# Performance work log

Hardware: AMD Instinct MI355X
Metric: run time of the kernel (lower is better)

## Reference

```python
import jax, jax.numpy as jnp
import numpy as np

HIDDEN = 1024
HEADS = 16
HEAD_DIM = HIDDEN // HEADS
FF = 4 * HIDDEN
B, S = 2, 2048


def _linear_params(key, out_dim, in_dim):
    kw, kb = jax.random.split(key)
    bound = 1.0 / np.sqrt(in_dim)
    W = jax.random.uniform(kw, (out_dim, in_dim), jnp.float32, -bound, bound)
    b = jax.random.uniform(kb, (out_dim,), jnp.float32, -bound, bound)
    return W, b


def setup_inputs() -> dict:
    key = jax.random.key(0)
    ks = jax.random.split(key, 8)
    x = jax.random.normal(ks[0], (B, S, HIDDEN), jnp.float32)
    attention_mask = jnp.ones((B, S), jnp.float32)
    Wq, bq = _linear_params(ks[1], HIDDEN, HIDDEN)
    Wk, bk = _linear_params(ks[2], HIDDEN, HIDDEN)
    Wv, bv = _linear_params(ks[3], HIDDEN, HIDDEN)
    Wo, bo = _linear_params(ks[4], HIDDEN, HIDDEN)
    W1, b1 = _linear_params(ks[5], FF, HIDDEN)
    W2, b2 = _linear_params(ks[6], HIDDEN, FF)
    g1 = jnp.ones((HIDDEN,), jnp.float32); be1 = jnp.zeros((HIDDEN,), jnp.float32)
    g2 = jnp.ones((HIDDEN,), jnp.float32); be2 = jnp.zeros((HIDDEN,), jnp.float32)
    return dict(x=x, attention_mask=attention_mask,
                Wq=Wq, bq=bq, Wk=Wk, bk=bk, Wv=Wv, bv=bv, Wo=Wo, bo=bo,
                W1=W1, b1=b1, W2=W2, b2=b2,
                g1=g1, be1=be1, g2=g2, be2=be2)


def _layer_norm(x, g, b, eps=1e-5):
    mu = jnp.mean(x, axis=-1, keepdims=True)
    var = jnp.mean(jnp.square(x - mu), axis=-1, keepdims=True)
    return (x - mu) * jax.lax.rsqrt(var + eps) * g + b


def reference(x, attention_mask, Wq, bq, Wk, bk, Wv, bv, Wo, bo,
              W1, b1, W2, b2, g1, be1, g2, be2):
    # Dropout is identity (eval mode / deterministic reference).
    residual = x
    h = _layer_norm(x, g1, be1)
    # [B,S,H] -> [B,nH,S,dh]
    def heads(t):
        return t.reshape(B, S, HEADS, HEAD_DIM).transpose(0, 2, 1, 3)
    q = heads(h @ Wq.T + bq)
    k = heads(h @ Wk.T + bk)
    v = heads(h @ Wv.T + bv)
    scores = jnp.einsum('bhqd,bhkd->bhqk', q, k) / np.sqrt(HEAD_DIM).astype(np.float32)
    scores = scores + (attention_mask[:, None, None, :] - 1.0) * 10000.0
    attn = jax.nn.softmax(scores, axis=-1)
    ctx = jnp.einsum('bhqk,bhkd->bhqd', attn, v)
    ctx = ctx.transpose(0, 2, 1, 3).reshape(B, S, HIDDEN)
    attn_out = ctx @ Wo.T + bo
    x = residual + attn_out
    residual = x
    h = _layer_norm(x, g2, be2)
    h = jax.nn.gelu(h @ W1.T + b1, approximate=False)
    h = h @ W2.T + b2
    return residual + h
```

## Files before the change

kernel.cpp:

```cpp
#include <hip/hip_runtime.h>
#include <hip/hip_bf16.h>
#include <math.h>

typedef __bf16 bf16;
typedef __bf16 bf16x4v __attribute__((ext_vector_type(4)));
typedef __bf16 bf16x8 __attribute__((ext_vector_type(8)));
typedef float  f32x4  __attribute__((ext_vector_type(4)));

#define HIDDEN 1024
#define TOKENS 4096
#define FFDIM  4096
#define SEQ    2048
#define NHEAD  16

#define LOG2E 1.44269504088896340736f

__device__ __forceinline__ void async_copy16(bf16* lds, const bf16* g)
{
    __builtin_amdgcn_global_load_lds(
        (__attribute__((address_space(1))) void*)g,
        (__attribute__((address_space(3))) void*)lds,
        16, 0, 0);
}

__global__ __launch_bounds__(256) void cvt_all_kernel(const float* __restrict__ wq,
    const float* __restrict__ wk, const float* __restrict__ wv, const float* __restrict__ wo,
    const float* __restrict__ w1, const float* __restrict__ w2, bf16* __restrict__ out)
{
    size_t i = ((size_t)blockIdx.x * 256 + threadIdx.x) * 4;
    int sel = (int)(i >> 20);
    const float* src;
    size_t off;
    if (sel < 4) { src = (sel == 0) ? wq : (sel == 1) ? wk : (sel == 2) ? wv : wo; off = i & ((1u << 20) - 1); }
    else if (sel < 8) { src = w1; off = i - ((size_t)4 << 20); }
    else              { src = w2; off = i - ((size_t)8 << 20); }
    float4 v = *(const float4*)&src[off];
    bf16x4v o = { (bf16)v.x, (bf16)v.y, (bf16)v.z, (bf16)v.w };
    *(bf16x4v*)&out[i] = o;
}

__global__ __launch_bounds__(256) void concat_bias_kernel(const float* __restrict__ bq,
    const float* __restrict__ bk, const float* __restrict__ bv, float* __restrict__ o)
{
    int i = blockIdx.x * 256 + threadIdx.x;
    float v = (i < 1024) ? bq[i] : (i < 2048 ? bk[i - 1024] : bv[i - 2048]);
    o[i] = v;
}

__global__ __launch_bounds__(256) void ln_kernel(const float* __restrict__ in,
    const float* __restrict__ g, const float* __restrict__ be, bf16* __restrict__ out)
{
    int row = blockIdx.x;
    int tid = threadIdx.x;
    const float* x = in + (size_t)row * HIDDEN;
    int i0 = tid * 4;
    float4 v = *(const float4*)&x[i0];
    float s  = v.x + v.y + v.z + v.w;
    float s2 = v.x*v.x + v.y*v.y + v.z*v.z + v.w*v.w;
    #pragma unroll
    for (int off = 32; off > 0; off >>= 1) { s += __shfl_xor(s, off); s2 += __shfl_xor(s2, off); }
    __shared__ float red[2][4];
    int wave = tid >> 6;
    if ((tid & 63) == 0) { red[0][wave] = s; red[1][wave] = s2; }
    __syncthreads();
    float ts  = red[0][0] + red[0][1] + red[0][2] + red[0][3];
    float ts2 = red[1][0] + red[1][1] + red[1][2] + red[1][3];
    float mu   = ts  * (1.0f / HIDDEN);
    float var  = ts2 * (1.0f / HIDDEN) - mu * mu;
    float rstd = rsqrtf(var + 1e-5f);
    float4 gg = *(const float4*)&g[i0];
    float4 bb = *(const float4*)&be[i0];
    bf16x4v o;
    o[0] = (bf16)((v.x - mu) * rstd * gg.x + bb.x);
    o[1] = (bf16)((v.y - mu) * rstd * gg.y + bb.y);
    o[2] = (bf16)((v.z - mu) * rstd * gg.z + bb.z);
    o[3] = (bf16)((v.w - mu) * rstd * gg.w + bb.w);
    *(bf16x4v*)&out[(size_t)row * HIDDEN + i0] = o;
}

template<int BM, int EPI, typename OT>
__global__ __launch_bounds__(256) void gemm_bt(const bf16* __restrict__ A, const bf16* __restrict__ Bt,
    const float* __restrict__ bias, const float* __restrict__ res, OT* __restrict__ C,
    int M, int N, int K)
{
    constexpr int MT = BM / 32;
    __shared__ bf16 As[BM * 64];
    __shared__ bf16 Bs[128 * 64];
    int tid  = threadIdx.x;
    int wave = tid >> 6, lane = tid & 63;
    int lm = lane & 15, quad = lane >> 4;
    int m0 = blockIdx.x * BM, n0 = blockIdx.y * 128;
    int wm = (wave >> 1) * (MT * 16), wn = (wave & 1) * 64;
    int r8 = lane >> 3, c8 = lane & 7;
    int gsw = (c8 ^ (r8 & 7)) * 8;
    f32x4 acc[MT][4] = {};
    for (int k0 = 0; k0 < K; k0 += 64) {
        #pragma unroll
        for (int ch = wave; ch < BM / 8; ch += 4)
            async_copy16(As + ch * 512, &A[(size_t)(m0 + ch * 8 + r8) * K + k0 + gsw]);
        #pragma unroll
        for (int ch = wave; ch < 16; ch += 4)
            async_copy16(Bs + ch * 512, &Bt[(size_t)(n0 + ch * 8 + r8) * K + k0 + gsw]);
        __syncthreads();
        bf16x8 af[MT][2], bfr[4][2];
        #pragma unroll
        for (int ks = 0; ks < 2; ks++) {
            int co = ((ks * 4 + quad) ^ (lm & 7)) * 8;
            #pragma unroll
            for (int t = 0; t < MT; t++) af[t][ks]  = *(const bf16x8*)&As[(wm + t * 16 + lm) * 64 + co];
            #pragma unroll
            for (int t = 0; t < 4; t++)  bfr[t][ks] = *(const bf16x8*)&Bs[(wn + t * 16 + lm) * 64 + co];
        }
        #pragma unroll
        for (int mt = 0; mt < MT; mt++)
            #pragma unroll
            for (int nt = 0; nt < 4; nt++)
                #pragma unroll
                for (int ks = 0; ks < 2; ks++)
                    acc[mt][nt] = __builtin_amdgcn_mfma_f32_16x16x32_bf16(af[mt][ks], bfr[nt][ks], acc[mt][nt], 0, 0, 0);
        __syncthreads();
    }
    #pragma unroll
    for (int mt = 0; mt < MT; mt++) {
        #pragma unroll
        for (int nt = 0; nt < 4; nt++) {
            int col = n0 + wn + nt * 16 + lm;
            float bv = bias[col];
            #pragma unroll
            for (int r = 0; r < 4; r++) {
                int row = m0 + wm + mt * 16 + quad * 4 + r;
                float vv = acc[mt][nt][r] + bv;
                if (EPI == 1) vv = 0.5f * vv * (1.0f + erff(vv * 0.70710678118654752f));
                if (EPI == 2) vv += res[(size_t)row * N + col];
                C[(size_t)row * N + col] = (OT)vv;
            }
        }
    }
}

__global__ __launch_bounds__(256) void gemm_qkv(const bf16* __restrict__ A, const bf16* __restrict__ W,
    const float* __restrict__ bias, bf16* __restrict__ qb, bf16* __restrict__ kb, bf16* __restrict__ vt)
{
    constexpr int K = HIDDEN;
    __shared__ bf16 As[128 * 64];
    __shared__ bf16 Bs[128 * 64];
    int tid  = threadIdx.x;
    int wave = tid >> 6, lane = tid & 63;
    int lm = lane & 15, quad = lane >> 4;
    int m0 = blockIdx.x * 128, n0 = blockIdx.y * 128;
    int wm = (wave >> 1) * 64, wn = (wave & 1) * 64;
    int r8 = lane >> 3, c8 = lane & 7;
    int gsw = (c8 ^ (r8 & 7)) * 8;
    f32x4 acc[4][4] = {};
    for (int k0 = 0; k0 < K; k0 += 64) {
        #pragma unroll
        for (int ch = wave; ch < 16; ch += 4) {
            async_copy16(As + ch * 512, &A[(size_t)(m0 + ch * 8 + r8) * K + k0 + gsw]);
            async_copy16(Bs + ch * 512, &W[(size_t)(n0 + ch * 8 + r8) * K + k0 + gsw]);
        }
        __syncthreads();
        bf16x8 af[4][2], bfr[4][2];
        #pragma unroll
        for (int ks = 0; ks < 2; ks++) {
            int co = ((ks * 4 + quad) ^ (lm & 7)) * 8;
            #pragma unroll
            for (int t = 0; t < 4; t++) {
                af[t][ks]  = *(const bf16x8*)&As[(wm + t * 16 + lm) * 64 + co];
                bfr[t][ks] = *(const bf16x8*)&Bs[(wn + t * 16 + lm) * 64 + co];
            }
        }
        #pragma unroll
        for (int mt = 0; mt < 4; mt++)
            #pragma unroll
            for (int nt = 0; nt < 4; nt++)
                #pragma unroll
                for (int ks = 0; ks < 2; ks++)
                    acc[mt][nt] = __builtin_amdgcn_mfma_f32_16x16x32_bf16(af[mt][ks], bfr[nt][ks], acc[mt][nt], 0, 0, 0);
        __syncthreads();
    }
    int region = n0 >> 10;
    #pragma unroll
    for (int mt = 0; mt < 4; mt++) {
        #pragma unroll
        for (int nt = 0; nt < 4; nt++) {
            int col = n0 + wn + nt * 16 + lm;
            float bv = bias[col];
            int cl = col & 1023;
            #pragma unroll
            for (int r = 0; r < 4; r++) {
                int row = m0 + wm + mt * 16 + quad * 4 + r;
                float vv = acc[mt][nt][r] + bv;
                if (region == 0)      qb[(size_t)row * HIDDEN + cl] = (bf16)vv;
                else if (region == 1) kb[(size_t)row * HIDDEN + cl] = (bf16)vv;
                else {
                    int h = cl >> 6, d = cl & 63;
                    int b = row >> 11, s = row & 2047;
                    vt[(((size_t)(b * NHEAD + h)) * 64 + d) * SEQ + s] = (bf16)vv;
                }
            }
        }
    }
}

__global__ __launch_bounds__(512, 8) void attn_kernel(const bf16* __restrict__ Q, const bf16* __restrict__ K,
    const bf16* __restrict__ Vt, const float* __restrict__ mask, bf16* __restrict__ O)
{
    __shared__ bf16 smem[20480];
    bf16* Ks0 = smem;
    bf16* Ks1 = smem + 4096;
    bf16* Vs0 = smem + 8192;
    bf16* Vs1 = smem + 12288;
    bf16* Ps  = smem + 16384;
    int tid = threadIdx.x, wave = tid >> 6, lane = tid & 63;
    int lm = lane & 15, quad = lane >> 4;
    int pair = wave >> 1, h = wave & 1;
    int bh = blockIdx.y, b = bh >> 4;
    int q0 = blockIdx.x * 64 + pair * 16;
    const size_t base  = ((size_t)b * SEQ) * HIDDEN + (bh & 15) * 64;
    const size_t vbase = (size_t)bh * 64 * SEQ;
    int srow8 = lane >> 3, spos = lane & 7;
    bf16x8 qf[2];
    #pragma unroll
    for (int ks = 0; ks < 2; ks++)
        qf[ks] = *(const bf16x8*)&Q[base + (size_t)(q0 + lm) * HIDDEN + ks * 32 + quad * 8];
    bf16x8 onesf;
    #pragma unroll
    for (int i = 0; i < 8; i++) onesf[i] = (bf16)1.0f;
    f32x4 o[4] = {};
    f32x4 lacc = {};
    const float c0 = 0.125f * LOG2E;
    const float cmk = 10000.0f * LOG2E;
    const float coff = -(cmk + 16.0f);
    bf16* pw = Ps + wave * 512;
    int r = wave * 8 + srow8;
    int gc = spos ^ (r & 7);
    auto stage = [&](bf16* kd, bf16* vd, int kt) {
        async_copy16(kd + wave * 512, &K [base  + (size_t)(kt + r) * HIDDEN + gc * 8]);
        async_copy16(vd + wave * 512, &Vt[vbase + (size_t)r * SEQ + kt + gc * 8]);
    };
    stage(Ks0, Vs0, 0);
    int kh = h * 32;
    for (int ti = 0; ti < SEQ / 64; ti++) {
        __syncthreads();
        const bf16* ksb = (ti & 1) ? Ks1 : Ks0;
        const bf16* vsb = (ti & 1) ? Vs1 : Vs0;
        if (ti + 1 < SEQ / 64) {
            if (ti & 1) stage(Ks0, Vs0, (ti + 1) * 64);
            else        stage(Ks1, Vs1, (ti + 1) * 64);
        }
        int kt = ti * 64;
        f32x4 st[2] = {};
        #pragma unroll
        for (int nt = 0; nt < 2; nt++) {
            #pragma unroll
            for (int ks = 0; ks < 2; ks++) {
                bf16x8 kf = *(const bf16x8*)&ksb[(kh + nt * 16 + lm) * 64 + (((ks * 4 + quad) ^ (lm & 7)) * 8)];
                st[nt] = __builtin_amdgcn_mfma_f32_16x16x32_bf16(kf, qf[ks], st[nt], 0, 0, 0);
            }
        }
        #pragma unroll
        for (int nt = 0; nt < 2; nt++) {
            float4 mv = *(const float4*)&mask[b * SEQ + kt + kh + nt * 16 + quad * 4];
            float p0 = __builtin_amdgcn_exp2f(st[nt][0] * c0 + (mv.x * cmk + coff));
            float p1 = __builtin_amdgcn_exp2f(st[nt][1] * c0 + (mv.y * cmk + coff));
            float p2 = __builtin_amdgcn_exp2f(st[nt][2] * c0 + (mv.z * cmk + coff));
            float p3 = __builtin_amdgcn_exp2f(st[nt][3] * c0 + (mv.w * cmk + coff));
            bf16x4v pk = { (bf16)p0, (bf16)p1, (bf16)p2, (bf16)p3 };
            *(bf16x4v*)&pw[lm * 32 + (((2 * nt + (quad >> 1)) ^ (lm & 3)) << 3) + ((quad & 1) << 2)] = pk;
        }
        bf16x8 pf = *(const bf16x8*)&pw[lm * 32 + ((quad ^ (lm & 3)) << 3)];
        lacc = __builtin_amdgcn_mfma_f32_16x16x32_bf16(pf, onesf, lacc, 0, 0, 0);
        #pragma unroll
        for (int dt = 0; dt < 4; dt++) {
            bf16x8 vf = *(const bf16x8*)&vsb[(dt * 16 + lm) * 64 + (((4 * h + quad) ^ (lm & 7)) * 8)];
            o[dt] = __builtin_amdgcn_mfma_f32_16x16x32_bf16(pf, vf, o[dt], 0, 0, 0);
        }
    }
    __syncthreads();
    float* scratch = (float*)smem;
    if (h == 1) {
        float* s = scratch + ((size_t)pair * 64 + lane) * 20;
        #pragma unroll
        for (int dt = 0; dt < 4; dt++) *(f32x4*)&s[dt * 4] = o[dt];
        *(f32x4*)&s[16] = lacc;
    }
    __syncthreads();
    if (h == 0) {
        const float* s = scratch + ((size_t)pair * 64 + lane) * 20;
        f32x4 po[4], pl;
        #pragma unroll
        for (int dt = 0; dt < 4; dt++) po[dt] = *(const f32x4*)&s[dt * 4];
        pl = *(const f32x4*)&s[16];
        #pragma unroll
        for (int rr = 0; rr < 4; rr++) {
            float inv = 1.0f / (lacc[rr] + pl[rr]);
            #pragma unroll
            for (int dt = 0; dt < 4; dt++) {
                float val = (o[dt][rr] + po[dt][rr]) * inv;
                O[base + (size_t)(q0 + quad * 4 + rr) * HIDDEN + dt * 16 + lm] = (bf16)val;
            }
        }
    }
}

extern "C" void kernel_launch(void* const* d_in, const int* in_sizes, int n_in,
                              void* d_out, int out_size, void* d_ws, size_t ws_size,
                              hipStream_t stream)
{
    (void)in_sizes; (void)n_in; (void)out_size; (void)ws_size;
    const float* x    = (const float*)d_in[0];
    const float* mask = (const float*)d_in[1];
    const float* Wq   = (const float*)d_in[2];
    const float* bq   = (const float*)d_in[3];
    const float* Wk   = (const float*)d_in[4];
    const float* bk   = (const float*)d_in[5];
    const float* Wv   = (const float*)d_in[6];
    const float* bv   = (const float*)d_in[7];
    const float* Wo   = (const float*)d_in[8];
    const float* bo   = (const float*)d_in[9];
    const float* W1   = (const float*)d_in[10];
    const float* b1   = (const float*)d_in[11];
    const float* W2   = (const float*)d_in[12];
    const float* b2   = (const float*)d_in[13];
    const float* g1   = (const float*)d_in[14];
    const float* be1  = (const float*)d_in[15];
    const float* g2   = (const float*)d_in[16];
    const float* be2  = (const float*)d_in[17];
    float* out = (float*)d_out;

    const size_t M1 = 1024u * 1024u;
    bf16* ws    = (bf16*)d_ws;
    bf16* Wqkv_b = ws;
    bf16* Wo_b  = ws + 3 * M1;
    bf16* W1_b  = ws + 4 * M1;
    bf16* W2_b  = ws + 8 * M1;
    bf16* qb    = ws + 12 * M1;
    bf16* kb    = ws + 16 * M1;
    bf16* vt    = ws + 20 * M1;
    bf16* cx    = ws + 24 * M1;
    bf16* h     = ws + 28 * M1;
    bf16* ffb   = ws + 12 * M1;
    float* biasqkv = (float*)(ws + 24 * M1);

    cvt_all_kernel<<<dim3(12288), 256, 0, stream>>>(Wq, Wk, Wv, Wo, W1, W2, Wqkv_b);
    concat_bias_kernel<<<dim3(12), 256, 0, stream>>>(bq, bk, bv, biasqkv);

    ln_kernel<<<dim3(TOKENS), 256, 0, stream>>>(x, g1, be1, h);
    gemm_qkv<<<dim3(32, 24), 256, 0, stream>>>(h, Wqkv_b, biasqkv, qb, kb, vt);
    attn_kernel<<<dim3(SEQ / 64, 32), 512, 0, stream>>>(qb, kb, vt, mask, cx);
    gemm_bt<64, 2, float><<<dim3(64, 8), 256, 0, stream>>>(cx, Wo_b, bo, x, out, TOKENS, HIDDEN, HIDDEN);
    ln_kernel<<<dim3(TOKENS), 256, 0, stream>>>(out, g2, be2, h);
    gemm_bt<128, 1, bf16><<<dim3(32, 32), 256, 0, stream>>>(h, W1_b, b1, nullptr, ffb, TOKENS, FFDIM, HIDDEN);
    gemm_bt<64, 2, float><<<dim3(64, 8), 256, 0, stream>>>(ffb, W2_b, b2, out, out, TOKENS, HIDDEN, FFDIM);
}
```

Before: 389.6 us.

## Process two query tiles per wave in attention and shuffle P via permlane

Each attention wave now handles 32 query rows instead of 16, reusing the loaded K and V fragments across two query tiles, and the grid is halved. The probability tile is rearranged into MFMA operand layout with permlane32_swap and shfl_xor, replacing the LDS store and reload, which frees the P buffer in shared memory. This trades higher register pressure (occupancy hint drops from 8 to 4) and fewer blocks for less LDS traffic per FLOP.

```diff
diff --git a/kernel.cpp b/kernel.cpp
--- a/kernel.cpp
+++ b/kernel.cpp
@@ -3,9 +3,12 @@
 #include <math.h>
 
 typedef __bf16 bf16;
+typedef __bf16 bf16x2 __attribute__((ext_vector_type(2)));
 typedef __bf16 bf16x4v __attribute__((ext_vector_type(4)));
 typedef __bf16 bf16x8 __attribute__((ext_vector_type(8)));
 typedef float  f32x4  __attribute__((ext_vector_type(4)));
+typedef unsigned u32x4 __attribute__((ext_vector_type(4)));
+typedef unsigned u32x2 __attribute__((ext_vector_type(2)));
 
 #define HIDDEN 1024
 #define TOKENS 4096
@@ -21,6 +24,18 @@
         (__attribute__((address_space(1))) void*)g,
         (__attribute__((address_space(3))) void*)lds,
         16, 0, 0);
+}
+
+__device__ __forceinline__ unsigned pack2(float lo, float hi)
+{
+    bf16x2 t; t[0] = (bf16)lo; t[1] = (bf16)hi;
+    return __builtin_bit_cast(unsigned, t);
+}
+
+__device__ __forceinline__ void pl32swap(unsigned& a, unsigned& b)
+{
+    u32x2 r = __builtin_amdgcn_permlane32_swap(a, b, false, false);
+    a = r.x; b = r.y;
 }
 
 __global__ __launch_bounds__(256) void cvt_all_kernel(const float* __restrict__ wq,
@@ -202,36 +217,36 @@
     }
 }
 
-__global__ __launch_bounds__(512, 8) void attn_kernel(const bf16* __restrict__ Q, const bf16* __restrict__ K,
+__global__ __launch_bounds__(512, 4) void attn_kernel(const bf16* __restrict__ Q, const bf16* __restrict__ K,
     const bf16* __restrict__ Vt, const float* __restrict__ mask, bf16* __restrict__ O)
 {
-    __shared__ bf16 smem[20480];
+    __shared__ bf16 smem[16384];
     bf16* Ks0 = smem;
     bf16* Ks1 = smem + 4096;
     bf16* Vs0 = smem + 8192;
     bf16* Vs1 = smem + 12288;
-    bf16* Ps  = smem + 16384;
     int tid = threadIdx.x, wave = tid >> 6, lane = tid & 63;
     int lm = lane & 15, quad = lane >> 4;
     int pair = wave >> 1, h = wave & 1;
     int bh = blockIdx.y, b = bh >> 4;
-    int q0 = blockIdx.x * 64 + pair * 16;
+    int q0 = blockIdx.x * 128 + pair * 32;
     const size_t base  = ((size_t)b * SEQ) * HIDDEN + (bh & 15) * 64;
     const size_t vbase = (size_t)bh * 64 * SEQ;
     int srow8 = lane >> 3, spos = lane & 7;
-    bf16x8 qf[2];
+    bf16x8 qf[2][2];
     #pragma unroll
-    for (int ks = 0; ks < 2; ks++)
-        qf[ks] = *(const bf16x8*)&Q[base + (size_t)(q0 + lm) * HIDDEN + ks * 32 + quad * 8];
+    for (int qt = 0; qt < 2; qt++)
+        #pragma unroll
+        for (int ks = 0; ks < 2; ks++)
+            qf[qt][ks] = *(const bf16x8*)&Q[base + (size_t)(q0 + qt * 16 + lm) * HIDDEN + ks * 32 + quad * 8];
     bf16x8 onesf;
     #pragma unroll
     for (int i = 0; i < 8; i++) onesf[i] = (bf16)1.0f;
-    f32x4 o[4] = {};
-    f32x4 lacc = {};
+    f32x4 o[2][4] = {};
+    f32x4 lacc[2] = {};
     const float c0 = 0.125f * LOG2E;
     const float cmk = 10000.0f * LOG2E;
     const float coff = -(cmk + 16.0f);
-    bf16* pw = Ps + wave * 512;
     int r = wave * 8 + srow8;
     int gc = spos ^ (r & 7);
     auto stage = [&](bf16* kd, bf16* vd, int kt) {
@@ -240,6 +255,7 @@
     };
     stage(Ks0, Vs0, 0);
     int kh = h * 32;
+    bool qodd = (quad & 1);
     for (int ti = 0; ti < SEQ / 64; ti++) {
         __syncthreads();
         const bf16* ksb = (ti & 1) ? Ks1 : Ks0;
@@ -249,55 +265,99 @@
             else        stage(Ks1, Vs1, (ti + 1) * 64);
         }
         int kt = ti * 64;
-        f32x4 st[2] = {};
-        #pragma unroll
-        for (int nt = 0; nt < 2; nt++) {
-            #pragma unroll
-            for (int ks = 0; ks < 2; ks++) {
-                bf16x8 kf = *(const bf16x8*)&ksb[(kh + nt * 16 + lm) * 64 + (((ks * 4 + quad) ^ (lm & 7)) * 8)];
-                st[nt] = __builtin_amdgcn_mfma_f32_16x16x32_bf16(kf, qf[ks], st[nt], 0, 0, 0);
-            }
-        }
+        bf16x8 kf[2][2];
+        #pragma unroll
+        for (int nt = 0; nt < 2; nt++)
+            #pragma unroll
+            for (int ks = 0; ks < 2; ks++)
+                kf[nt][ks] = *(const bf16x8*)&ksb[(kh + nt * 16 + lm) * 64 + (((ks * 4 + quad) ^ (lm & 7)) * 8)];
+        f32x4 st[2][2] = {};
+        #pragma unroll
+        for (int qt = 0; qt < 2; qt++)
+            #pragma unroll
+            for (int nt = 0; nt < 2; nt++)
+                #pragma unroll
+                for (int ks = 0; ks < 2; ks++)
+                    st[qt][nt] = __builtin_amdgcn_mfma_f32_16x16x32_bf16(kf[nt][ks], qf[qt][ks], st[qt][nt], 0, 0, 0);
+        float madd[2][4];
         #pragma unroll
         for (int nt = 0; nt < 2; nt++) {
             float4 mv = *(const float4*)&mask[b * SEQ + kt + kh + nt * 16 + quad * 4];
-            float p0 = __builtin_amdgcn_exp2f(st[nt][0] * c0 + (mv.x * cmk + coff));
-            float p1 = __builtin_amdgcn_exp2f(st[nt][1] * c0 + (mv.y * cmk + coff));
-            float p2 = __builtin_amdgcn_exp2f(st[nt][2] * c0 + (mv.z * cmk + coff));
-            float p3 = __builtin_amdgcn_exp2f(st[nt][3] * c0 + (mv.w * cmk + coff));
-            bf16x4v pk = { (bf16)p0, (bf16)p1, (bf16)p2, (bf16)p3 };
-            *(bf16x4v*)&pw[lm * 32 + (((2 * nt + (quad >> 1)) ^ (lm & 3)) << 3) + ((quad & 1) << 2)] = pk;
-        }
-        bf16x8 pf = *(const bf16x8*)&pw[lm * 32 + ((quad ^ (lm & 3)) << 3)];
-        lacc = __builtin_amdgcn_mfma_f32_16x16x32_bf16(pf, onesf, lacc, 0, 0, 0);
+            madd[nt][0] = mv.x * cmk + coff; madd[nt][1] = mv.y * cmk + coff;
+            madd[nt][2] = mv.z * cmk + coff; madd[nt][3] = mv.w * cmk + coff;
+        }
+        bf16x8 af[2];
+        #pragma unroll
+        for (int qt = 0; qt < 2; qt++) {
+            unsigned w[2][2];
+            #pragma unroll
+            for (int nt = 0; nt < 2; nt++) {
+                float p0 = __builtin_amdgcn_exp2f(st[qt][nt][0] * c0 + madd[nt][0]);
+                float p1 = __builtin_amdgcn_exp2f(st[qt][nt][1] * c0 + madd[nt][1]);
+                float p2 = __builtin_amdgcn_exp2f(st[qt][nt][2] * c0 + madd[nt][2]);
+                float p3 = __builtin_amdgcn_exp2f(st[qt][nt][3] * c0 + madd[nt][3]);
+                w[nt][0] = pack2(p0, p1);
+                w[nt][1] = pack2(p2, p3);
+            }
+            unsigned A0 = w[0][0], B0 = w[1][0];
+            unsigned A1 = w[0][1], B1 = w[1][1];
+            pl32swap(A0, B0);
+            pl32swap(A1, B1);
+            unsigned F0 = __shfl_xor(A0, 16), G0 = __shfl_xor(B0, 16);
+            unsigned F1 = __shfl_xor(A1, 16), G1 = __shfl_xor(B1, 16);
+            u32x4 uu;
+            uu.x = qodd ? G0 : A0;
+            uu.y = qodd ? G1 : A1;
+            uu.z = qodd ? B0 : F0;
+            uu.w = qodd ? B1 : F1;
+            af[qt] = __builtin_bit_cast(bf16x8, uu);
+            lacc[qt] = __builtin_amdgcn_mfma_f32_16x16x32_bf16(af[qt], onesf, lacc[qt], 0, 0, 0);
+        }
         #pragma unroll
         for (int dt = 0; dt < 4; dt++) {
             bf16x8 vf = *(const bf16x8*)&vsb[(dt * 16 + lm) * 64 + (((4 * h + quad) ^ (lm & 7)) * 8)];
-            o[dt] = __builtin_amdgcn_mfma_f32_16x16x32_bf16(pf, vf, o[dt], 0, 0, 0);
+            #pragma unroll
+            for (int qt = 0; qt < 2; qt++)
+                o[qt][dt] = __builtin_amdgcn_mfma_f32_16x16x32_bf16(af[qt], vf, o[qt][dt], 0, 0, 0);
         }
     }
     __syncthreads();
     float* scratch = (float*)smem;
+    float* s = scratch + ((size_t)pair * 64 + lane) * 20;
     if (h == 1) {
-        float* s = scratch + ((size_t)pair * 64 + lane) * 20;
-        #pragma unroll
-        for (int dt = 0; dt < 4; dt++) *(f32x4*)&s[dt * 4] = o[dt];
-        *(f32x4*)&s[16] = lacc;
+        #pragma unroll
+        for (int dt = 0; dt < 4; dt++) *(f32x4*)&s[dt * 4] = o[0][dt];
+        *(f32x4*)&s[16] = lacc[0];
     }
     __syncthreads();
     if (h == 0) {
-        const float* s = scratch + ((size_t)pair * 64 + lane) * 20;
-        f32x4 po[4], pl;
-        #pragma unroll
-        for (int dt = 0; dt < 4; dt++) po[dt] = *(const f32x4*)&s[dt * 4];
-        pl = *(const f32x4*)&s[16];
+        f32x4 pl = *(const f32x4*)&s[16];
         #pragma unroll
         for (int rr = 0; rr < 4; rr++) {
-            float inv = 1.0f / (lacc[rr] + pl[rr]);
+            float inv = 1.0f / (lacc[0][rr] + pl[rr]);
             #pragma unroll
             for (int dt = 0; dt < 4; dt++) {
-                float val = (o[dt][rr] + po[dt][rr]) * inv;
+                float val = (o[0][dt][rr] + s[dt * 4 + rr]) * inv;
                 O[base + (size_t)(q0 + quad * 4 + rr) * HIDDEN + dt * 16 + lm] = (bf16)val;
+            }
+        }
+    }
+    __syncthreads();
+    if (h == 0) {
+        #pragma unroll
+        for (int dt = 0; dt < 4; dt++) *(f32x4*)&s[dt * 4] = o[1][dt];
+        *(f32x4*)&s[16] = lacc[1];
+    }
+    __syncthreads();
+    if (h == 1) {
+        f32x4 pl = *(const f32x4*)&s[16];
+        #pragma unroll
+        for (int rr = 0; rr < 4; rr++) {
+            float inv = 1.0f / (lacc[1][rr] + pl[rr]);
+            #pragma unroll
+            for (int dt = 0; dt < 4; dt++) {
+                float val = (o[1][dt][rr] + s[dt * 4 + rr]) * inv;
+                O[base + (size_t)(q0 + 16 + quad * 4 + rr) * HIDDEN + dt * 16 + lm] = (bf16)val;
             }
         }
     }
@@ -347,7 +407,7 @@
 
     ln_kernel<<<dim3(TOKENS), 256, 0, stream>>>(x, g1, be1, h);
     gemm_qkv<<<dim3(32, 24), 256, 0, stream>>>(h, Wqkv_b, biasqkv, qb, kb, vt);
-    attn_kernel<<<dim3(SEQ / 64, 32), 512, 0, stream>>>(qb, kb, vt, mask, cx);
+    attn_kernel<<<dim3(SEQ / 128, 32), 512, 0, stream>>>(qb, kb, vt, mask, cx);
     gemm_bt<64, 2, float><<<dim3(64, 8), 256, 0, stream>>>(cx, Wo_b, bo, x, out, TOKENS, HIDDEN, HIDDEN);
     ln_kernel<<<dim3(TOKENS), 256, 0, stream>>>(out, g2, be2, h);
     gemm_bt<128, 1, bf16><<<dim3(32, 32), 256, 0, stream>>>(h, W1_b, b1, nullptr, ffb, TOKENS, FFDIM, HIDDEN);
```

New measurement: 370.9 us. 4.8% less time.
